# Kernel optimization log

Measured on AMD Instinct MI355X. Metric: run time of the kernel, lower is better.

## Reference

```python
import jax, jax.numpy as jnp
import numpy as np

B, NPG, FANOUT = 32, 1024, 4       # graphs, nodes per graph, tree fan-out
H = 128                            # x_size == h_size
NUM_LAYERS = 4
A, BCAPS = 8, 8                    # TreeCaps a, b
DCC, N_CLASSES = 16, 50
ROUTING_ITER = 3
TYPE_VOCAB, TOKEN_VOCAB = 1000, 30000
EPS = 1e-10


def _build_forest():
    # parent of node i (i>0) is (i-1)//FANOUT; node 0 is root. Same tree per graph.
    child = np.arange(1, NPG)
    parent = (child - 1) // FANOUT
    pos = ((child - 1) % FANOUT).astype(np.float32)           # position in parent's mailbox
    cnt = np.bincount(parent, minlength=NPG).astype(np.float32)
    k = cnt[parent]                                           # child count of each edge's parent
    denom = np.maximum(k - 1.0, 1.0)
    lw = np.where(k == 1.0, 1.0, (k - 1.0 - pos) / denom).astype(np.float32)
    rw = np.where(k == 1.0, 0.0, pos / denom).astype(np.float32)
    offs = (np.arange(B) * NPG)[:, None]
    src = (child[None, :] + offs).reshape(-1).astype(np.int32)
    dst = (parent[None, :] + offs).reshape(-1).astype(np.int32)
    return src, dst, np.tile(lw, B), np.tile(rw, B), np.tile(cnt > 0, B)


def setup_inputs() -> dict:
    key = jax.random.key(0)
    ks = jax.random.split(key, 9)
    src, dst, lw, rw, has_children = _build_forest()
    N = B * NPG
    u = lambda k, s: jax.random.uniform(k, s, jnp.float32, -0.1, 0.1)
    return {
        "type_ids": jax.random.randint(ks[0], (N,), 0, TYPE_VOCAB, dtype=jnp.int32),
        "token_ids": jax.random.randint(ks[1], (N,), 0, TOKEN_VOCAB, dtype=jnp.int32),
        "src": jnp.asarray(src), "dst": jnp.asarray(dst),
        "lw": jnp.asarray(lw), "rw": jnp.asarray(rw),
        "has_children": jnp.asarray(has_children),
        "type_emb": jax.random.normal(ks[2], (TYPE_VOCAB, H - H // 2), jnp.float32),
        "token_emb": jax.random.normal(ks[3], (TOKEN_VOCAB, H // 2), jnp.float32),
        "W_left": u(ks[4], (NUM_LAYERS, H, H)),
        "W_right": u(ks[5], (NUM_LAYERS, H, H)),
        "W_top": u(ks[6], (NUM_LAYERS, H, H)),
        "b_conv": u(ks[7], (NUM_LAYERS, H)),
        "Wjm": 0.01 * jax.random.normal(ks[8], (A * H, DCC, N_CLASSES, NUM_LAYERS), jnp.float32),
    }


def squash(x, axis=-1):
    sq = jnp.sum(x * x, axis=axis, keepdims=True)
    return x * (sq / (1.0 + sq) / (jnp.sqrt(sq + EPS) + 1e-8))


def _vts_routing(uu):
    # uu: [NPG, H, L]  (one graph's primary capsules)
    l2 = jnp.sum(uu.reshape(NPG, -1) ** 2, axis=1)
    _, top_b = jax.lax.top_k(l2, BCAPS)
    u_i = jax.lax.stop_gradient(uu[top_b].reshape(-1, NUM_LAYERS))  # [BCAPS*H, L]
    _, top_a = jax.lax.top_k(l2, A)
    v_j = uu[top_a].reshape(-1, NUM_LAYERS)                         # [A*H, L]
    alpha = jnp.zeros((BCAPS * H, A * H), uu.dtype)
    for _ in range(ROUTING_ITER):
        alpha = alpha + u_i @ v_j.T
        beta = jax.nn.softmax(alpha, axis=-1)
        v_j = beta.T @ u_i
    return squash(v_j)                                              # [A*H, L]


def _dynamic_routing(SC, Wjm):
    # SC: [B, A*H, L], Wjm: [A*H, DCC, S, L]
    v = jnp.einsum('ncsm,bnm->bnsc', Wjm, SC)
    v_stop = jax.lax.stop_gradient(v)
    delta = jnp.zeros(SC.shape[:2] + (N_CLASSES,), SC.dtype)
    z = None
    for r in range(ROUTING_ITER):
        gamma = jax.nn.softmax(delta, axis=-1)
        vv = v if r == ROUTING_ITER - 1 else v_stop
        z = squash(jnp.einsum('bns,bnsc->bsc', gamma, vv))
        if r < ROUTING_ITER - 1:
            delta = delta + jnp.einsum('bnsc,bsc->bns', v_stop, z)
    return z                                                        # [B, S, DCC]


def reference(type_ids, token_ids, src, dst, lw, rw, has_children,
              type_emb, token_emb, W_left, W_right, W_top, b_conv, Wjm):
    h = jnp.concatenate([type_emb[type_ids], token_emb[token_ids]], axis=1)  # [N, H]
    N = h.shape[0]
    feats = []
    for l in range(NUM_LAYERS):
        ch = h[src]                                                 # [E, H] gather children
        msg = (ch @ W_left[l]) * lw[:, None] + (ch @ W_right[l]) * rw[:, None]
        children = jax.ops.segment_sum(msg, dst, num_segments=N)
        new_h = jax.nn.relu(children + h @ W_top[l] + b_conv[l][None, :])
        h = jnp.where(has_children[:, None], new_h, h)              # leaves keep old h
        feats.append(h)
    layer_feats = jnp.stack(feats, axis=-1)                         # [N, H, L]
    SC = jax.vmap(_vts_routing)(layer_feats.reshape(B, NPG, H, NUM_LAYERS))
    z = _dynamic_routing(SC, Wjm)
    logit = jnp.sqrt(jnp.sum(z * z, axis=-1) + EPS)                 # [B, S]
    return (logit, logit)
```

## Files before the change

kernel.cpp:

```cpp
#include <hip/hip_runtime.h>


#define BG      32
#define NPG     1024
#define HH      128
#define NLAY    4
#define INT_PG  256
#define M_INT   8192
#define NN      32768
#define EPG     1023
#define DCC     16
#define NS      50

__global__ void k_embed(const int* __restrict__ tids, const int* __restrict__ kids,
                        const float* __restrict__ temb, const float* __restrict__ kemb,
                        float* __restrict__ hA, float* __restrict__ hB) {
  int idx = blockIdx.x * 256 + threadIdx.x;
  int n = idx >> 5, c4 = idx & 31;
  float4 v;
  if (c4 < 16) v = *(const float4*)(temb + tids[n] * 64 + c4 * 4);
  else         v = *(const float4*)(kemb + kids[n] * 64 + (c4 - 16) * 4);
  *(float4*)(hA + n * 128 + c4 * 4) = v;
  if ((n & 1023) >= INT_PG)
    *(float4*)(hB + n * 128 + c4 * 4) = v;
}

__global__ __launch_bounds__(256) void k_conv(
    const float* __restrict__ hp, float* __restrict__ hn,
    const int* __restrict__ src, const float* __restrict__ lw,
    const float* __restrict__ rw,
    const float* __restrict__ Wl, const float* __restrict__ Wr,
    const float* __restrict__ Wt, const float* __restrict__ bias,
    float* __restrict__ feat) {
  __shared__ float Ws[2][32][128];
  __shared__ float AsT[2][32][20];
  __shared__ float hlS[16][128];
  __shared__ float hrS[16][128];
  int tid = threadIdx.x;
  int tx = tid & 31, ty = tid >> 5;
  int rowBase = blockIdx.x * 16;
  int g = rowBase >> 8, plBase = rowBase & 255;
  int nodeBase = g * NPG + plBase;

  #pragma unroll
  for (int t = 0; t < 2; ++t) {
    int it = t * 256 + tid;
    int pw = it >> 5, c4 = it & 31;
    int pl = plBase + pw;
    float4 al = make_float4(0.f, 0.f, 0.f, 0.f);
    float4 ar = make_float4(0.f, 0.f, 0.f, 0.f);
    #pragma unroll
    for (int j = 0; j < 4; ++j) {
      int cc = 4 * pl + 1 + j;
      if (cc < NPG) {
        int e = g * EPG + cc - 1;
        int child = src[e];
        float lv = lw[e], rv = rw[e];
        float4 hv = *(const float4*)(hp + child * 128 + c4 * 4);
        al.x = fmaf(lv, hv.x, al.x); al.y = fmaf(lv, hv.y, al.y);
        al.z = fmaf(lv, hv.z, al.z); al.w = fmaf(lv, hv.w, al.w);
        ar.x = fmaf(rv, hv.x, ar.x); ar.y = fmaf(rv, hv.y, ar.y);
        ar.z = fmaf(rv, hv.z, ar.z); ar.w = fmaf(rv, hv.w, ar.w);
      }
    }
    *(float4*)&hlS[pw][c4 * 4] = al;
    *(float4*)&hrS[pw][c4 * 4] = ar;
  }
  __syncthreads();

  float acc[2][4] = {};
  int sr = tid >> 3, sc4 = (tid & 7) * 4;

  {
    float4 av = make_float4(0.f, 0.f, 0.f, 0.f);
    if (tid < 128) av = *(const float4*)&hlS[sr][sc4];
    const float* wsrc = Wl;
    int f0 = tid, f1 = tid + 256, f2 = tid + 512, f3 = tid + 768;
    float4 wv0 = *(const float4*)(wsrc + (f0 >> 5) * 128 + (f0 & 31) * 4);
    float4 wv1 = *(const float4*)(wsrc + (f1 >> 5) * 128 + (f1 & 31) * 4);
    float4 wv2 = *(const float4*)(wsrc + (f2 >> 5) * 128 + (f2 & 31) * 4);
    float4 wv3 = *(const float4*)(wsrc + (f3 >> 5) * 128 + (f3 & 31) * 4);
    if (tid < 128) {
      AsT[0][sc4 + 0][sr] = av.x; AsT[0][sc4 + 1][sr] = av.y;
      AsT[0][sc4 + 2][sr] = av.z; AsT[0][sc4 + 3][sr] = av.w;
    }
    *(float4*)&Ws[0][f0 >> 5][(f0 & 31) * 4] = wv0;
    *(float4*)&Ws[0][f1 >> 5][(f1 & 31) * 4] = wv1;
    *(float4*)&Ws[0][f2 >> 5][(f2 & 31) * 4] = wv2;
    *(float4*)&Ws[0][f3 >> 5][(f3 & 31) * 4] = wv3;
  }
  __syncthreads();

  for (int kc = 0; kc < 12; ++kc) {
    int cur = kc & 1, nxt = cur ^ 1;
    if (kc < 11) {
      int kc1 = kc + 1;
      int ssel = kc1 >> 2, kcol = (kc1 & 3) * 32;
      float4 av = make_float4(0.f, 0.f, 0.f, 0.f);
      if (tid < 128) {
        if (ssel == 0)      av = *(const float4*)&hlS[sr][kcol + sc4];
        else if (ssel == 1) av = *(const float4*)&hrS[sr][kcol + sc4];
        else                av = *(const float4*)(hp + (nodeBase + sr) * 128 + kcol + sc4);
      }
      const float* wsrc = ((ssel == 0) ? Wl : (ssel == 1) ? Wr : Wt) + kcol * 128;
      int f0 = tid, f1 = tid + 256, f2 = tid + 512, f3 = tid + 768;
      float4 wv0 = *(const float4*)(wsrc + (f0 >> 5) * 128 + (f0 & 31) * 4);
      float4 wv1 = *(const float4*)(wsrc + (f1 >> 5) * 128 + (f1 & 31) * 4);
      float4 wv2 = *(const float4*)(wsrc + (f2 >> 5) * 128 + (f2 & 31) * 4);
      float4 wv3 = *(const float4*)(wsrc + (f3 >> 5) * 128 + (f3 & 31) * 4);
      if (tid < 128) {
        AsT[nxt][sc4 + 0][sr] = av.x; AsT[nxt][sc4 + 1][sr] = av.y;
        AsT[nxt][sc4 + 2][sr] = av.z; AsT[nxt][sc4 + 3][sr] = av.w;
      }
      *(float4*)&Ws[nxt][f0 >> 5][(f0 & 31) * 4] = wv0;
      *(float4*)&Ws[nxt][f1 >> 5][(f1 & 31) * 4] = wv1;
      *(float4*)&Ws[nxt][f2 >> 5][(f2 & 31) * 4] = wv2;
      *(float4*)&Ws[nxt][f3 >> 5][(f3 & 31) * 4] = wv3;
    }
    #pragma unroll
    for (int kk = 0; kk < 32; ++kk) {
      float4 wv = *(float4*)&Ws[cur][kk][tx * 4];
      float2 av2 = *(float2*)&AsT[cur][kk][ty * 2];
      float aa[2] = {av2.x, av2.y};
      float ww[4] = {wv.x, wv.y, wv.z, wv.w};
      #pragma unroll
      for (int i = 0; i < 2; ++i)
        #pragma unroll
        for (int j = 0; j < 4; ++j)
          acc[i][j] = fmaf(aa[i], ww[j], acc[i][j]);
    }
    if (kc != 11) __syncthreads();
  }
  float4 bv = *(const float4*)(bias + tx * 4);
  float bb[4] = {bv.x, bv.y, bv.z, bv.w};
  #pragma unroll
  for (int i = 0; i < 2; ++i) {
    int r = ty * 2 + i;
    float4 o = make_float4(fmaxf(acc[i][0] + bb[0], 0.f),
                           fmaxf(acc[i][1] + bb[1], 0.f),
                           fmaxf(acc[i][2] + bb[2], 0.f),
                           fmaxf(acc[i][3] + bb[3], 0.f));
    *(float4*)(feat + (rowBase + r) * 128 + tx * 4) = o;
    *(float4*)(hn + (nodeBase + r) * 128 + tx * 4) = o;
  }
}

__global__ void k_l2(const float* __restrict__ h, const float* __restrict__ feat,
                     float* __restrict__ l2) {
  int wid = (blockIdx.x * 256 + threadIdx.x) >> 6;
  int lane = threadIdx.x & 63;
  int g = wid >> 10, local = wid & 1023;
  float s = 0.f;
  if (local >= INT_PG) {
    const float* p = h + wid * 128;
    float a = p[lane], b = p[lane + 64];
    s = (a * a + b * b) * 4.f;
  } else {
    int row = (g * INT_PG + local) * 128;
    #pragma unroll
    for (int l = 0; l < 4; ++l) {
      const float* p = feat + l * (M_INT * 128) + row;
      float a = p[lane], b = p[lane + 64];
      s += a * a + b * b;
    }
  }
  #pragma unroll
  for (int off = 32; off; off >>= 1) s += __shfl_down(s, off);
  if (lane == 0) l2[wid] = s;
}

__global__ __launch_bounds__(256) void k_topsel(const float* __restrict__ l2,
                                                const float* __restrict__ h,
                                                const float* __restrict__ feat,
                                                float* __restrict__ U,
                                                float* __restrict__ Vsum) {
  __shared__ int ssel[8];
  int g = blockIdx.x, tid = threadIdx.x;
  int lane = tid & 63;
  if (tid < 64) {
    unsigned long long kk[16];
    #pragma unroll
    for (int k = 0; k < 16; ++k) {
      int i = k * 64 + lane;
      unsigned vb = __float_as_uint(l2[g * 1024 + i]);
      kk[k] = ((unsigned long long)vb << 32) | (unsigned)(~i);
    }
    for (int r = 0; r < 8; ++r) {
      unsigned long long best = 0ULL;
      #pragma unroll
      for (int k = 0; k < 16; ++k) best = (kk[k] > best) ? kk[k] : best;
      #pragma unroll
      for (int off = 32; off; off >>= 1) {
        unsigned long long o = __shfl_down(best, off);
        best = (o > best) ? o : best;
      }
      best = __shfl(best, 0);
      if (lane == 0) ssel[r] = (int)(~(unsigned)(best & 0xffffffffu));
      #pragma unroll
      for (int k = 0; k < 16; ++k) if (kk[k] == best) kk[k] = 0ULL;
    }
  }
  __syncthreads();
  for (int t = 0; t < 4; ++t) {
    int idx = t * 256 + tid;
    int rank = idx >> 7, hh = idx & 127;
    int local = ssel[rank];
    float4 v;
    if (local >= INT_PG) {
      float x = h[(g * NPG + local) * 128 + hh];
      v = make_float4(x, x, x, x);
    } else {
      int row = (g * INT_PG + local) * 128 + hh;
      v.x = feat[row];
      v.y = feat[M_INT * 128 + row];
      v.z = feat[2 * M_INT * 128 + row];
      v.w = feat[3 * M_INT * 128 + row];
    }
    int o = g * 1024 + rank * 128 + hh;
    ((float4*)U)[o] = v;
    ((float4*)Vsum)[o] = v;
  }
}

__global__ __launch_bounds__(1024) void k_vtsA(const float* __restrict__ U,
                                               const float* __restrict__ Vsum,
                                               float* __restrict__ mw, float* __restrict__ sw) {
  __shared__ float4 Vs2[64 * 17];
  int g = blockIdx.x >> 4, rb = (blockIdx.x & 15) * 64;
  int tid = threadIdx.x, p = tid & 15, r = tid >> 4;
  Vs2[(tid & 63) * 17 + (tid >> 6)] = ((const float4*)Vsum)[g * 1024 + tid];
  __syncthreads();
  float4 u = ((const float4*)U)[g * 1024 + rb + r];
  float m = -3.4e38f;
  for (int i = 0; i < 64; ++i) {
    float4 v = Vs2[i * 17 + p];
    float a = u.x * v.x + u.y * v.y + u.z * v.z + u.w * v.w;
    m = fmaxf(m, a);
  }
  #pragma unroll
  for (int mk = 8; mk; mk >>= 1) m = fmaxf(m, __shfl_xor(m, mk));
  float s = 0.f;
  for (int i = 0; i < 64; ++i) {
    float4 v = Vs2[i * 17 + p];
    float a = u.x * v.x + u.y * v.y + u.z * v.z + u.w * v.w;
    s += __expf(a - m);
  }
  #pragma unroll
  for (int mk = 8; mk; mk >>= 1) s += __shfl_xor(s, mk);
  if (p == 0) {
    mw[g * 1024 + rb + r] = m;
    sw[g * 1024 + rb + r] = s;
  }
}

__global__ __launch_bounds__(1024) void k_vtsB(const float* __restrict__ U,
                                               float* __restrict__ Vsum,
                                               const float* __restrict__ mw,
                                               const float* __restrict__ sw,
                                               float* __restrict__ SCT, int last) {
  __shared__ float4 Us2[64 * 17];
  __shared__ float2 Ms2[64 * 17];
  int g = blockIdx.x >> 4, cb = (blockIdx.x & 15) * 64;
  int tid = threadIdx.x, p = tid & 15, q = tid >> 4;
  Us2[(tid & 63) * 17 + (tid >> 6)] = ((const float4*)U)[g * 1024 + tid];
  Ms2[(tid & 63) * 17 + (tid >> 6)] =
      make_float2(mw[g * 1024 + tid], 1.0f / sw[g * 1024 + tid]);
  __syncthreads();
  float4 v = ((const float4*)Vsum)[g * 1024 + cb + q];
  float4 acc = make_float4(0.f, 0.f, 0.f, 0.f);
  for (int i = 0; i < 64; ++i) {
    float4 uu = Us2[i * 17 + p];
    float2 st = Ms2[i * 17 + p];
    float a = uu.x * v.x + uu.y * v.y + uu.z * v.z + uu.w * v.w;
    float w = __expf(a - st.x) * st.y;
    acc.x = fmaf(w, uu.x, acc.x); acc.y = fmaf(w, uu.y, acc.y);
    acc.z = fmaf(w, uu.z, acc.z); acc.w = fmaf(w, uu.w, acc.w);
  }
  #pragma unroll
  for (int mk = 8; mk; mk >>= 1) {
    acc.x += __shfl_xor(acc.x, mk);
    acc.y += __shfl_xor(acc.y, mk);
    acc.z += __shfl_xor(acc.z, mk);
    acc.w += __shfl_xor(acc.w, mk);
  }
  if (p == 0) {
    float4 o = acc;
    int jc = cb + q;
    if (last) {
      float sq = o.x * o.x + o.y * o.y + o.z * o.z + o.w * o.w;
      float f = (sq / (1.f + sq)) / (sqrtf(sq + 1e-10f) + 1e-8f);
      ((float4*)SCT)[jc * 32 + g] = make_float4(o.x * f, o.y * f, o.z * f, o.w * f);
    } else {
      float4 w0 = ((const float4*)Vsum)[g * 1024 + jc];
      ((float4*)Vsum)[g * 1024 + jc] = make_float4(w0.x + o.x, w0.y + o.y,
                                                   w0.z + o.z, w0.w + o.w);
    }
  }
}

__global__ void k_transW(const float* __restrict__ Wjm, float* __restrict__ WT) {
  __shared__ float w[3200];
  int n = blockIdx.x, tid = threadIdx.x;
  for (int i = tid; i < 3200; i += 256) w[i] = Wjm[n * 3200 + i];
  __syncthreads();
  for (int i = tid; i < 3200; i += 256) {
    int s = i >> 6, cm = i & 63;
    int cc = cm >> 2, m = cm & 3;
    WT[(s * 1024 + n) * 64 + cm] = w[(cc * NS + s) * 4 + m];
  }
}

__global__ __launch_bounds__(256) void k_zsweep(const float* __restrict__ WT,
                                                const float* __restrict__ SCT,
                                                const float* __restrict__ gT,
                                                float* __restrict__ zpart, int it0) {
  int sb = blockIdx.x >> 4, nb = blockIdx.x & 15;
  int tid = threadIdx.x;
  int b = tid & 31, ch = tid >> 5;
  int n0 = nb * 64;
  const float4* wt = (const float4*)WT + (sb * 1024 + n0) * 16;
  const float4* sct = (const float4*)SCT + n0 * 32 + b;
  const float* gp = gT + (sb * 1024 + n0) * 32 + b;
  float a0 = 0.f, a1 = 0.f;
  #pragma unroll 8
  for (int nn = 0; nn < 64; ++nn) {
    float4 w0 = wt[nn * 16 + ch];
    float4 w1 = wt[nn * 16 + ch + 8];
    float4 s4 = sct[nn * 32];
    float gm = it0 ? (1.0f / 50.0f) : gp[nn * 32];
    float t0 = w0.x * s4.x + w0.y * s4.y + w0.z * s4.z + w0.w * s4.w;
    float t1 = w1.x * s4.x + w1.y * s4.y + w1.z * s4.z + w1.w * s4.w;
    a0 = fmaf(gm, t0, a0);
    a1 = fmaf(gm, t1, a1);
  }
  zpart[blockIdx.x * 512 + tid] = a0;
  zpart[blockIdx.x * 512 + 256 + tid] = a1;
}

__global__ void k_zred(const float* __restrict__ zpart, float* __restrict__ accZ) {
  int idx = blockIdx.x * 256 + threadIdx.x;
  if (idx >= 25600) return;
  int c = idx & 15;
  int sb = (idx >> 4) % NS;
  int b = idx / (16 * NS);
  int lofs = (c < 8) ? (c * 32 + b) : (256 + (c - 8) * 32 + b);
  const float* zp = zpart + sb * 16 * 512 + lofs;
  float s = 0.f;
  #pragma unroll
  for (int nb = 0; nb < 16; ++nb) s += zp[nb * 512];
  accZ[idx] = s;
}

__global__ void k_logits(const float* __restrict__ accZ, float* __restrict__ out) {
  int idx = blockIdx.x * 256 + threadIdx.x;
  if (idx >= 1600) return;
  const float4* a4 = (const float4*)accZ + idx * 4;
  float4 u0 = a4[0], u1 = a4[1], u2 = a4[2], u3 = a4[3];
  float sq = u0.x * u0.x + u0.y * u0.y + u0.z * u0.z + u0.w * u0.w
           + u1.x * u1.x + u1.y * u1.y + u1.z * u1.z + u1.w * u1.w
           + u2.x * u2.x + u2.y * u2.y + u2.z * u2.z + u2.w * u2.w
           + u3.x * u3.x + u3.y * u3.y + u3.z * u3.z + u3.w * u3.w;
  float f = (sq / (1.f + sq)) / (sqrtf(sq + 1e-10f) + 1e-8f);
  float lg = sqrtf(sq * f * f + 1e-10f);
  out[idx] = lg;
  out[idx + 1600] = lg;
}

__global__ __launch_bounds__(256) void k_dsweep(const float* __restrict__ WT,
                                                const float* __restrict__ SCT,
                                                const float* __restrict__ accZ,
                                                float* __restrict__ delta,
                                                float* __restrict__ gT, int first) {
  __shared__ float wl[50 * 64];
  __shared__ float4 scl[32];
  __shared__ float dtot[NS][32];
  __shared__ float mb[32], ib[32];
  int n = blockIdx.x;
  int tid = threadIdx.x;
  for (int i = tid; i < 3200; i += 256)
    wl[i] = WT[((i >> 6) * 1024 + n) * 64 + (i & 63)];
  if (tid < 32) scl[tid] = ((const float4*)SCT)[n * 32 + tid];
  __syncthreads();
  for (int idx = tid; idx < 1600; idx += 256) {
    int s = idx >> 5, b = idx & 31;
    const float4* wp = (const float4*)(wl + s * 64);
    const float4* zp = (const float4*)(accZ + (b * 50 + s) * 16);
    float4 u0 = zp[0], u1 = zp[1], u2 = zp[2], u3 = zp[3];
    float sq = u0.x * u0.x + u0.y * u0.y + u0.z * u0.z + u0.w * u0.w
             + u1.x * u1.x + u1.y * u1.y + u1.z * u1.z + u1.w * u1.w
             + u2.x * u2.x + u2.y * u2.y + u2.z * u2.z + u2.w * u2.w
             + u3.x * u3.x + u3.y * u3.y + u3.z * u3.z + u3.w * u3.w;
    float f = (sq / (1.f + sq)) / (sqrtf(sq + 1e-10f) + 1e-8f);
    float zs[16] = {u0.x * f, u0.y * f, u0.z * f, u0.w * f,
                    u1.x * f, u1.y * f, u1.z * f, u1.w * f,
                    u2.x * f, u2.y * f, u2.z * f, u2.w * f,
                    u3.x * f, u3.y * f, u3.z * f, u3.w * f};
    float4 y = make_float4(0.f, 0.f, 0.f, 0.f);
    #pragma unroll
    for (int c = 0; c < 16; ++c) {
      float4 w = wp[c];
      float zc = zs[c];
      y.x = fmaf(zc, w.x, y.x); y.y = fmaf(zc, w.y, y.y);
      y.z = fmaf(zc, w.z, y.z); y.w = fmaf(zc, w.w, y.w);
    }
    float4 sc = scl[b];
    float dd = sc.x * y.x + sc.y * y.y + sc.z * y.z + sc.w * y.w;
    float dt = first ? dd : (delta[(s * 1024 + n) * 32 + b] + dd);
    dtot[s][b] = dt;
    if (first) delta[(s * 1024 + n) * 32 + b] = dt;
  }
  __syncthreads();
  if (tid < 32) {
    float m = -3.4e38f;
    for (int s = 0; s < NS; ++s) m = fmaxf(m, dtot[s][tid]);
    float sum = 0.f;
    for (int s = 0; s < NS; ++s) sum += __expf(dtot[s][tid] - m);
    mb[tid] = m; ib[tid] = 1.0f / sum;
  }
  __syncthreads();
  for (int idx = tid; idx < 1600; idx += 256) {
    int s = idx >> 5, b = idx & 31;
    gT[(s * 1024 + n) * 32 + b] = __expf(dtot[s][b] - mb[b]) * ib[b];
  }
}

extern "C" void kernel_launch(void* const* d_in, const int* in_sizes, int n_in,
                              void* d_out, int out_size, void* d_ws, size_t ws_size,
                              hipStream_t stream) {
  const int*   type_ids  = (const int*)d_in[0];
  const int*   token_ids = (const int*)d_in[1];
  const int*   src       = (const int*)d_in[2];
  const float* lw        = (const float*)d_in[4];
  const float* rw        = (const float*)d_in[5];
  const float* temb      = (const float*)d_in[7];
  const float* kemb      = (const float*)d_in[8];
  const float* Wl        = (const float*)d_in[9];
  const float* Wr        = (const float*)d_in[10];
  const float* Wt        = (const float*)d_in[11];
  const float* bconv     = (const float*)d_in[12];
  const float* Wjm       = (const float*)d_in[13];
  float* out = (float*)d_out;
  char* wsb = (char*)d_ws;

  float* hA    = (float*)(wsb + 0);
  float* hB    = (float*)(wsb + 16777216);
  float* feat  = (float*)(wsb + 33554432);
  float* WT    = (float*)(wsb + 50331648);
  float* delta = (float*)(wsb + 63438848);
  float* gT    = (float*)(wsb + 69992448);
  float* accZ  = (float*)(wsb + 76546048);
  float* l2b   = (float*)(wsb + 76853248);
  float* U     = (float*)(wsb + 76984320);
  float* Vsum  = (float*)(wsb + 77508608);
  float* mw    = (float*)(wsb + 78032896);
  float* sw    = (float*)(wsb + 78163968);
  float* SCT   = (float*)(wsb + 78295040);
  float* zpart = (float*)(wsb + 78819328);

  k_embed<<<4096, 256, 0, stream>>>(type_ids, token_ids, temb, kemb, hA, hB);
  k_transW<<<1024, 256, 0, stream>>>(Wjm, WT);

  for (int l = 0; l < NLAY; ++l) {
    const float* hp = (l & 1) ? hB : hA;
    float*       hn = (l & 1) ? hA : hB;
    k_conv<<<512, 256, 0, stream>>>(hp, hn, src, lw, rw,
                                    Wl + l * 16384, Wr + l * 16384, Wt + l * 16384,
                                    bconv + l * 128, feat + l * (M_INT * 128));
  }

  k_l2<<<8192, 256, 0, stream>>>(hA, feat, l2b);
  k_topsel<<<32, 256, 0, stream>>>(l2b, hA, feat, U, Vsum);

  for (int it = 0; it < 3; ++it) {
    k_vtsA<<<512, 1024, 0, stream>>>(U, Vsum, mw, sw);
    k_vtsB<<<512, 1024, 0, stream>>>(U, Vsum, mw, sw, SCT, it == 2 ? 1 : 0);
  }

  for (int it = 0; it < 3; ++it) {
    k_zsweep<<<800, 256, 0, stream>>>(WT, SCT, gT, zpart, it == 0 ? 1 : 0);
    k_zred<<<100, 256, 0, stream>>>(zpart, accZ);
    if (it < 2)
      k_dsweep<<<1024, 256, 0, stream>>>(WT, SCT, accZ, delta, gT, it == 0 ? 1 : 0);
  }
  k_logits<<<7, 256, 0, stream>>>(accZ, out);
}
```

Before: 432.0 us.

## Merge init kernels, register-block VTS routing, fuse squash and logits into reduction

Merges the embedding gather and the Wjm transpose into a single launch. The VTS routing kernels drop from 1024 to 256 threads per block, and each thread now handles four rows or columns, so every value read from shared memory is reused across four dot products. The squash step is moved into k_zred, which also writes the logits on the last iteration; this removes k_logits and the per-block squash recomputation in k_dsweep. The aim is fewer launches and less redundant work, at the cost of higher register pressure in the VTS kernels.

```diff
diff --git a/kernel.cpp b/kernel.cpp
--- a/kernel.cpp
+++ b/kernel.cpp
@@ -12,17 +12,31 @@
 #define DCC     16
 #define NS      50
 
-__global__ void k_embed(const int* __restrict__ tids, const int* __restrict__ kids,
-                        const float* __restrict__ temb, const float* __restrict__ kemb,
-                        float* __restrict__ hA, float* __restrict__ hB) {
-  int idx = blockIdx.x * 256 + threadIdx.x;
-  int n = idx >> 5, c4 = idx & 31;
-  float4 v;
-  if (c4 < 16) v = *(const float4*)(temb + tids[n] * 64 + c4 * 4);
-  else         v = *(const float4*)(kemb + kids[n] * 64 + (c4 - 16) * 4);
-  *(float4*)(hA + n * 128 + c4 * 4) = v;
-  if ((n & 1023) >= INT_PG)
-    *(float4*)(hB + n * 128 + c4 * 4) = v;
+__global__ void k_init(const int* __restrict__ tids, const int* __restrict__ kids,
+                       const float* __restrict__ temb, const float* __restrict__ kemb,
+                       float* __restrict__ hA, float* __restrict__ hB,
+                       const float* __restrict__ Wjm, float* __restrict__ WT) {
+  __shared__ float w[3200];
+  int tid = threadIdx.x;
+  if (blockIdx.x < 4096) {
+    int idx = blockIdx.x * 256 + tid;
+    int n = idx >> 5, c4 = idx & 31;
+    float4 v;
+    if (c4 < 16) v = *(const float4*)(temb + tids[n] * 64 + c4 * 4);
+    else         v = *(const float4*)(kemb + kids[n] * 64 + (c4 - 16) * 4);
+    *(float4*)(hA + n * 128 + c4 * 4) = v;
+    if ((n & 1023) >= INT_PG)
+      *(float4*)(hB + n * 128 + c4 * 4) = v;
+  } else {
+    int n = blockIdx.x - 4096;
+    for (int i = tid; i < 3200; i += 256) w[i] = Wjm[n * 3200 + i];
+    __syncthreads();
+    for (int i = tid; i < 3200; i += 256) {
+      int s = i >> 6, cm = i & 63;
+      int cc = cm >> 2, m = cm & 3;
+      WT[(s * 1024 + n) * 64 + cm] = w[(cc * NS + s) * 4 + m];
+    }
+  }
 }
 
 __global__ __launch_bounds__(256) void k_conv(
@@ -222,91 +236,138 @@
   }
 }
 
-__global__ __launch_bounds__(1024) void k_vtsA(const float* __restrict__ U,
-                                               const float* __restrict__ Vsum,
-                                               float* __restrict__ mw, float* __restrict__ sw) {
+__global__ __launch_bounds__(256) void k_vtsA(const float* __restrict__ U,
+                                              const float* __restrict__ Vsum,
+                                              float* __restrict__ mw, float* __restrict__ sw) {
   __shared__ float4 Vs2[64 * 17];
   int g = blockIdx.x >> 4, rb = (blockIdx.x & 15) * 64;
-  int tid = threadIdx.x, p = tid & 15, r = tid >> 4;
-  Vs2[(tid & 63) * 17 + (tid >> 6)] = ((const float4*)Vsum)[g * 1024 + tid];
-  __syncthreads();
-  float4 u = ((const float4*)U)[g * 1024 + rb + r];
-  float m = -3.4e38f;
+  int tid = threadIdx.x, p = tid & 15, rg = tid >> 4;
+  #pragma unroll
+  for (int t = 0; t < 4; ++t) {
+    int j = t * 256 + tid;
+    Vs2[(j & 63) * 17 + (j >> 6)] = ((const float4*)Vsum)[g * 1024 + j];
+  }
+  __syncthreads();
+  int r0 = rb + rg * 4;
+  float4 u0 = ((const float4*)U)[g * 1024 + r0 + 0];
+  float4 u1 = ((const float4*)U)[g * 1024 + r0 + 1];
+  float4 u2 = ((const float4*)U)[g * 1024 + r0 + 2];
+  float4 u3 = ((const float4*)U)[g * 1024 + r0 + 3];
+  float m0 = -3.4e38f, m1 = -3.4e38f, m2 = -3.4e38f, m3 = -3.4e38f;
   for (int i = 0; i < 64; ++i) {
     float4 v = Vs2[i * 17 + p];
-    float a = u.x * v.x + u.y * v.y + u.z * v.z + u.w * v.w;
-    m = fmaxf(m, a);
-  }
-  #pragma unroll
-  for (int mk = 8; mk; mk >>= 1) m = fmaxf(m, __shfl_xor(m, mk));
-  float s = 0.f;
+    float a0 = u0.x * v.x + u0.y * v.y + u0.z * v.z + u0.w * v.w;
+    float a1 = u1.x * v.x + u1.y * v.y + u1.z * v.z + u1.w * v.w;
+    float a2 = u2.x * v.x + u2.y * v.y + u2.z * v.z + u2.w * v.w;
+    float a3 = u3.x * v.x + u3.y * v.y + u3.z * v.z + u3.w * v.w;
+    m0 = fmaxf(m0, a0); m1 = fmaxf(m1, a1);
+    m2 = fmaxf(m2, a2); m3 = fmaxf(m3, a3);
+  }
+  #pragma unroll
+  for (int mk = 8; mk; mk >>= 1) {
+    m0 = fmaxf(m0, __shfl_xor(m0, mk));
+    m1 = fmaxf(m1, __shfl_xor(m1, mk));
+    m2 = fmaxf(m2, __shfl_xor(m2, mk));
+    m3 = fmaxf(m3, __shfl_xor(m3, mk));
+  }
+  float s0 = 0.f, s1 = 0.f, s2 = 0.f, s3 = 0.f;
   for (int i = 0; i < 64; ++i) {
     float4 v = Vs2[i * 17 + p];
-    float a = u.x * v.x + u.y * v.y + u.z * v.z + u.w * v.w;
-    s += __expf(a - m);
-  }
-  #pragma unroll
-  for (int mk = 8; mk; mk >>= 1) s += __shfl_xor(s, mk);
+    float a0 = u0.x * v.x + u0.y * v.y + u0.z * v.z + u0.w * v.w;
+    float a1 = u1.x * v.x + u1.y * v.y + u1.z * v.z + u1.w * v.w;
+    float a2 = u2.x * v.x + u2.y * v.y + u2.z * v.z + u2.w * v.w;
+    float a3 = u3.x * v.x + u3.y * v.y + u3.z * v.z + u3.w * v.w;
+    s0 += __expf(a0 - m0); s1 += __expf(a1 - m1);
+    s2 += __expf(a2 - m2); s3 += __expf(a3 - m3);
+  }
+  #pragma unroll
+  for (int mk = 8; mk; mk >>= 1) {
+    s0 += __shfl_xor(s0, mk);
+    s1 += __shfl_xor(s1, mk);
+    s2 += __shfl_xor(s2, mk);
+    s3 += __shfl_xor(s3, mk);
+  }
   if (p == 0) {
-    mw[g * 1024 + rb + r] = m;
-    sw[g * 1024 + rb + r] = s;
-  }
-}
-
-__global__ __launch_bounds__(1024) void k_vtsB(const float* __restrict__ U,
-                                               float* __restrict__ Vsum,
-                                               const float* __restrict__ mw,
-                                               const float* __restrict__ sw,
-                                               float* __restrict__ SCT, int last) {
+    mw[g * 1024 + r0 + 0] = m0; sw[g * 1024 + r0 + 0] = s0;
+    mw[g * 1024 + r0 + 1] = m1; sw[g * 1024 + r0 + 1] = s1;
+    mw[g * 1024 + r0 + 2] = m2; sw[g * 1024 + r0 + 2] = s2;
+    mw[g * 1024 + r0 + 3] = m3; sw[g * 1024 + r0 + 3] = s3;
+  }
+}
+
+__global__ __launch_bounds__(256) void k_vtsB(const float* __restrict__ U,
+                                              float* __restrict__ Vsum,
+                                              const float* __restrict__ mw,
+                                              const float* __restrict__ sw,
+                                              float* __restrict__ SCT, int last) {
   __shared__ float4 Us2[64 * 17];
   __shared__ float2 Ms2[64 * 17];
   int g = blockIdx.x >> 4, cb = (blockIdx.x & 15) * 64;
-  int tid = threadIdx.x, p = tid & 15, q = tid >> 4;
-  Us2[(tid & 63) * 17 + (tid >> 6)] = ((const float4*)U)[g * 1024 + tid];
-  Ms2[(tid & 63) * 17 + (tid >> 6)] =
-      make_float2(mw[g * 1024 + tid], 1.0f / sw[g * 1024 + tid]);
-  __syncthreads();
-  float4 v = ((const float4*)Vsum)[g * 1024 + cb + q];
-  float4 acc = make_float4(0.f, 0.f, 0.f, 0.f);
+  int tid = threadIdx.x, p = tid & 15, qg = tid >> 4;
+  #pragma unroll
+  for (int t = 0; t < 4; ++t) {
+    int j = t * 256 + tid;
+    Us2[(j & 63) * 17 + (j >> 6)] = ((const float4*)U)[g * 1024 + j];
+    Ms2[(j & 63) * 17 + (j >> 6)] =
+        make_float2(mw[g * 1024 + j], 1.0f / sw[g * 1024 + j]);
+  }
+  __syncthreads();
+  int c0 = cb + qg * 4;
+  float4 v0 = ((const float4*)Vsum)[g * 1024 + c0 + 0];
+  float4 v1 = ((const float4*)Vsum)[g * 1024 + c0 + 1];
+  float4 v2 = ((const float4*)Vsum)[g * 1024 + c0 + 2];
+  float4 v3 = ((const float4*)Vsum)[g * 1024 + c0 + 3];
+  float4 acc0 = make_float4(0.f, 0.f, 0.f, 0.f);
+  float4 acc1 = make_float4(0.f, 0.f, 0.f, 0.f);
+  float4 acc2 = make_float4(0.f, 0.f, 0.f, 0.f);
+  float4 acc3 = make_float4(0.f, 0.f, 0.f, 0.f);
   for (int i = 0; i < 64; ++i) {
     float4 uu = Us2[i * 17 + p];
     float2 st = Ms2[i * 17 + p];
-    float a = uu.x * v.x + uu.y * v.y + uu.z * v.z + uu.w * v.w;
-    float w = __expf(a - st.x) * st.y;
-    acc.x = fmaf(w, uu.x, acc.x); acc.y = fmaf(w, uu.y, acc.y);
-    acc.z = fmaf(w, uu.z, acc.z); acc.w = fmaf(w, uu.w, acc.w);
+    float a0 = uu.x * v0.x + uu.y * v0.y + uu.z * v0.z + uu.w * v0.w;
+    float a1 = uu.x * v1.x + uu.y * v1.y + uu.z * v1.z + uu.w * v1.w;
+    float a2 = uu.x * v2.x + uu.y * v2.y + uu.z * v2.z + uu.w * v2.w;
+    float a3 = uu.x * v3.x + uu.y * v3.y + uu.z * v3.z + uu.w * v3.w;
+    float w0 = __expf(a0 - st.x) * st.y;
+    float w1 = __expf(a1 - st.x) * st.y;
+    float w2 = __expf(a2 - st.x) * st.y;
+    float w3 = __expf(a3 - st.x) * st.y;
+    acc0.x = fmaf(w0, uu.x, acc0.x); acc0.y = fmaf(w0, uu.y, acc0.y);
+    acc0.z = fmaf(w0, uu.z, acc0.z); acc0.w = fmaf(w0, uu.w, acc0.w);
+    acc1.x = fmaf(w1, uu.x, acc1.x); acc1.y = fmaf(w1, uu.y, acc1.y);
+    acc1.z = fmaf(w1, uu.z, acc1.z); acc1.w = fmaf(w1, uu.w, acc1.w);
+    acc2.x = fmaf(w2, uu.x, acc2.x); acc2.y = fmaf(w2, uu.y, acc2.y);
+    acc2.z = fmaf(w2, uu.z, acc2.z); acc2.w = fmaf(w2, uu.w, acc2.w);
+    acc3.x = fmaf(w3, uu.x, acc3.x); acc3.y = fmaf(w3, uu.y, acc3.y);
+    acc3.z = fmaf(w3, uu.z, acc3.z); acc3.w = fmaf(w3, uu.w, acc3.w);
   }
   #pragma unroll
   for (int mk = 8; mk; mk >>= 1) {
-    acc.x += __shfl_xor(acc.x, mk);
-    acc.y += __shfl_xor(acc.y, mk);
-    acc.z += __shfl_xor(acc.z, mk);
-    acc.w += __shfl_xor(acc.w, mk);
+    acc0.x += __shfl_xor(acc0.x, mk); acc0.y += __shfl_xor(acc0.y, mk);
+    acc0.z += __shfl_xor(acc0.z, mk); acc0.w += __shfl_xor(acc0.w, mk);
+    acc1.x += __shfl_xor(acc1.x, mk); acc1.y += __shfl_xor(acc1.y, mk);
+    acc1.z += __shfl_xor(acc1.z, mk); acc1.w += __shfl_xor(acc1.w, mk);
+    acc2.x += __shfl_xor(acc2.x, mk); acc2.y += __shfl_xor(acc2.y, mk);
+    acc2.z += __shfl_xor(acc2.z, mk); acc2.w += __shfl_xor(acc2.w, mk);
+    acc3.x += __shfl_xor(acc3.x, mk); acc3.y += __shfl_xor(acc3.y, mk);
+    acc3.z += __shfl_xor(acc3.z, mk); acc3.w += __shfl_xor(acc3.w, mk);
   }
   if (p == 0) {
-    float4 o = acc;
-    int jc = cb + q;
-    if (last) {
-      float sq = o.x * o.x + o.y * o.y + o.z * o.z + o.w * o.w;
-      float f = (sq / (1.f + sq)) / (sqrtf(sq + 1e-10f) + 1e-8f);
-      ((float4*)SCT)[jc * 32 + g] = make_float4(o.x * f, o.y * f, o.z * f, o.w * f);
-    } else {
-      float4 w0 = ((const float4*)Vsum)[g * 1024 + jc];
-      ((float4*)Vsum)[g * 1024 + jc] = make_float4(w0.x + o.x, w0.y + o.y,
-                                                   w0.z + o.z, w0.w + o.w);
-    }
-  }
-}
-
-__global__ void k_transW(const float* __restrict__ Wjm, float* __restrict__ WT) {
-  __shared__ float w[3200];
-  int n = blockIdx.x, tid = threadIdx.x;
-  for (int i = tid; i < 3200; i += 256) w[i] = Wjm[n * 3200 + i];
-  __syncthreads();
-  for (int i = tid; i < 3200; i += 256) {
-    int s = i >> 6, cm = i & 63;
-    int cc = cm >> 2, m = cm & 3;
-    WT[(s * 1024 + n) * 64 + cm] = w[(cc * NS + s) * 4 + m];
+    float4 oo[4] = {acc0, acc1, acc2, acc3};
+    #pragma unroll
+    for (int k = 0; k < 4; ++k) {
+      float4 o = oo[k];
+      int jc = c0 + k;
+      if (last) {
+        float sq = o.x * o.x + o.y * o.y + o.z * o.z + o.w * o.w;
+        float f = (sq / (1.f + sq)) / (sqrtf(sq + 1e-10f) + 1e-8f);
+        ((float4*)SCT)[jc * 32 + g] = make_float4(o.x * f, o.y * f, o.z * f, o.w * f);
+      } else {
+        float4 w0 = ((const float4*)Vsum)[g * 1024 + jc];
+        ((float4*)Vsum)[g * 1024 + jc] = make_float4(w0.x + o.x, w0.y + o.y,
+                                                     w0.z + o.z, w0.w + o.w);
+      }
+    }
   }
 }
 
@@ -337,38 +398,45 @@
   zpart[blockIdx.x * 512 + 256 + tid] = a1;
 }
 
-__global__ void k_zred(const float* __restrict__ zpart, float* __restrict__ accZ) {
-  int idx = blockIdx.x * 256 + threadIdx.x;
-  if (idx >= 25600) return;
+__global__ void k_zred(const float* __restrict__ zpart, float* __restrict__ z,
+                       float* __restrict__ out, int last) {
+  __shared__ float sb_[256];
+  __shared__ float fb[16];
+  __shared__ float sqb[16];
+  int tid = threadIdx.x;
+  int idx = blockIdx.x * 256 + tid;
   int c = idx & 15;
-  int sb = (idx >> 4) % NS;
+  int sbk = (idx >> 4) % NS;
   int b = idx / (16 * NS);
   int lofs = (c < 8) ? (c * 32 + b) : (256 + (c - 8) * 32 + b);
-  const float* zp = zpart + sb * 16 * 512 + lofs;
+  const float* zp = zpart + sbk * 16 * 512 + lofs;
   float s = 0.f;
   #pragma unroll
   for (int nb = 0; nb < 16; ++nb) s += zp[nb * 512];
-  accZ[idx] = s;
-}
-
-__global__ void k_logits(const float* __restrict__ accZ, float* __restrict__ out) {
-  int idx = blockIdx.x * 256 + threadIdx.x;
-  if (idx >= 1600) return;
-  const float4* a4 = (const float4*)accZ + idx * 4;
-  float4 u0 = a4[0], u1 = a4[1], u2 = a4[2], u3 = a4[3];
-  float sq = u0.x * u0.x + u0.y * u0.y + u0.z * u0.z + u0.w * u0.w
-           + u1.x * u1.x + u1.y * u1.y + u1.z * u1.z + u1.w * u1.w
-           + u2.x * u2.x + u2.y * u2.y + u2.z * u2.z + u2.w * u2.w
-           + u3.x * u3.x + u3.y * u3.y + u3.z * u3.z + u3.w * u3.w;
-  float f = (sq / (1.f + sq)) / (sqrtf(sq + 1e-10f) + 1e-8f);
-  float lg = sqrtf(sq * f * f + 1e-10f);
-  out[idx] = lg;
-  out[idx + 1600] = lg;
+  sb_[tid] = s;
+  __syncthreads();
+  if ((tid & 15) == 0) {
+    float sq = 0.f;
+    #pragma unroll
+    for (int cc = 0; cc < 16; ++cc) sq += sb_[tid + cc] * sb_[tid + cc];
+    float f = (sq / (1.f + sq)) / (sqrtf(sq + 1e-10f) + 1e-8f);
+    fb[tid >> 4] = f;
+    sqb[tid >> 4] = sq;
+  }
+  __syncthreads();
+  z[idx] = s * fb[tid >> 4];
+  if (last && (tid & 15) == 0) {
+    float sq = sqb[tid >> 4], f = fb[tid >> 4];
+    float lg = sqrtf(sq * f * f + 1e-10f);
+    int pr = idx >> 4;
+    out[pr] = lg;
+    out[pr + 1600] = lg;
+  }
 }
 
 __global__ __launch_bounds__(256) void k_dsweep(const float* __restrict__ WT,
                                                 const float* __restrict__ SCT,
-                                                const float* __restrict__ accZ,
+                                                const float* __restrict__ z,
                                                 float* __restrict__ delta,
                                                 float* __restrict__ gT, int first) {
   __shared__ float wl[50 * 64];
@@ -384,17 +452,10 @@
   for (int idx = tid; idx < 1600; idx += 256) {
     int s = idx >> 5, b = idx & 31;
     const float4* wp = (const float4*)(wl + s * 64);
-    const float4* zp = (const float4*)(accZ + (b * 50 + s) * 16);
-    float4 u0 = zp[0], u1 = zp[1], u2 = zp[2], u3 = zp[3];
-    float sq = u0.x * u0.x + u0.y * u0.y + u0.z * u0.z + u0.w * u0.w
-             + u1.x * u1.x + u1.y * u1.y + u1.z * u1.z + u1.w * u1.w
-             + u2.x * u2.x + u2.y * u2.y + u2.z * u2.z + u2.w * u2.w
-             + u3.x * u3.x + u3.y * u3.y + u3.z * u3.z + u3.w * u3.w;
-    float f = (sq / (1.f + sq)) / (sqrtf(sq + 1e-10f) + 1e-8f);
-    float zs[16] = {u0.x * f, u0.y * f, u0.z * f, u0.w * f,
-                    u1.x * f, u1.y * f, u1.z * f, u1.w * f,
-                    u2.x * f, u2.y * f, u2.z * f, u2.w * f,
-                    u3.x * f, u3.y * f, u3.z * f, u3.w * f};
+    const float4* zp = (const float4*)(z + (b * 50 + s) * 16);
+    float4 z0 = zp[0], z1 = zp[1], z2 = zp[2], z3 = zp[3];
+    float zs[16] = {z0.x, z0.y, z0.z, z0.w, z1.x, z1.y, z1.z, z1.w,
+                    z2.x, z2.y, z2.z, z2.w, z3.x, z3.y, z3.z, z3.w};
     float4 y = make_float4(0.f, 0.f, 0.f, 0.f);
     #pragma unroll
     for (int c = 0; c < 16; ++c) {
@@ -448,7 +509,7 @@
   float* WT    = (float*)(wsb + 50331648);
   float* delta = (float*)(wsb + 63438848);
   float* gT    = (float*)(wsb + 69992448);
-  float* accZ  = (float*)(wsb + 76546048);
+  float* z     = (float*)(wsb + 76546048);
   float* l2b   = (float*)(wsb + 76853248);
   float* U     = (float*)(wsb + 76984320);
   float* Vsum  = (float*)(wsb + 77508608);
@@ -457,8 +518,8 @@
   float* SCT   = (float*)(wsb + 78295040);
   float* zpart = (float*)(wsb + 78819328);
 
-  k_embed<<<4096, 256, 0, stream>>>(type_ids, token_ids, temb, kemb, hA, hB);
-  k_transW<<<1024, 256, 0, stream>>>(Wjm, WT);
+  k_init<<<5120, 256, 0, stream>>>(type_ids, token_ids, temb, kemb, hA, hB,
+                                   Wjm, WT);
 
   for (int l = 0; l < NLAY; ++l) {
     const float* hp = (l & 1) ? hB : hA;
@@ -472,15 +533,14 @@
   k_topsel<<<32, 256, 0, stream>>>(l2b, hA, feat, U, Vsum);
 
   for (int it = 0; it < 3; ++it) {
-    k_vtsA<<<512, 1024, 0, stream>>>(U, Vsum, mw, sw);
-    k_vtsB<<<512, 1024, 0, stream>>>(U, Vsum, mw, sw, SCT, it == 2 ? 1 : 0);
+    k_vtsA<<<512, 256, 0, stream>>>(U, Vsum, mw, sw);
+    k_vtsB<<<512, 256, 0, stream>>>(U, Vsum, mw, sw, SCT, it == 2 ? 1 : 0);
   }
 
   for (int it = 0; it < 3; ++it) {
     k_zsweep<<<800, 256, 0, stream>>>(WT, SCT, gT, zpart, it == 0 ? 1 : 0);
-    k_zred<<<100, 256, 0, stream>>>(zpart, accZ);
+    k_zred<<<100, 256, 0, stream>>>(zpart, z, out, it == 2 ? 1 : 0);
     if (it < 2)
-      k_dsweep<<<1024, 256, 0, stream>>>(WT, SCT, accZ, delta, gT, it == 0 ? 1 : 0);
-  }
-  k_logits<<<7, 256, 0, stream>>>(accZ, out);
-}
+      k_dsweep<<<1024, 256, 0, stream>>>(WT, SCT, z, delta, gT, it == 0 ? 1 : 0);
+  }
+}
```

Measured after the change: 468.5 us. +8.5%, slower.
